# Kernel optimization log

Hardware: AMD Instinct MI355X
Metric: run time of the kernel (lower is better)

The kernel has to match this reference:

```python
import math
import jax, jax.numpy as jnp
import numpy as np

B, CIN, COUT, K, Z, H, W = 8, 512, 512, 3, 512, 64, 64


def setup_inputs() -> dict:
    key = jax.random.key(0)
    k1, k2, k3, k4 = jax.random.split(key, 4)
    inp = {
        "input": jax.random.normal(k1, (B, CIN, H, W), dtype=jnp.float32),
        "style": jax.random.normal(k2, (B, Z), dtype=jnp.float32),
        # base conv weight: [1, out, in, k, k]
        "weight": jax.random.normal(k3, (1, COUT, CIN, K, K), dtype=jnp.float32),
        # EqualLinear modulation params (lr_mul=1, bias_init=1)
        "mod_w": jax.random.normal(k4, (CIN, Z), dtype=jnp.float32),
        "mod_b": jnp.ones((CIN,), dtype=jnp.float32),
    }
    return inp


def reference(input, style, weight, mod_w, mod_b):
    # EqualLinear: scale = 1/sqrt(z_dim), lr_mul = 1, no activation
    z_dim = mod_w.shape[1]
    mod_scale = 1.0 / math.sqrt(z_dim)
    s = style @ (mod_w * mod_scale).T + mod_b  # [B, in]

    # modulated per-sample weights: scale * base_weight * style
    in_ch, k = weight.shape[2], weight.shape[-1]
    conv_scale = 1.0 / math.sqrt(in_ch * k * k)
    w = conv_scale * weight * s[:, None, :, None, None]  # [B, out, in, k, k]

    pad = k // 2

    def conv_one(x, wb):  # x: [in, H, W], wb: [out, in, k, k]
        return jax.lax.conv_general_dilated(
            x[None], wb, window_strides=(1, 1),
            padding=[(pad, pad), (pad, pad)],
            dimension_numbers=("NCHW", "OIHW", "NCHW"),
        )[0]

    out = jax.vmap(conv_one)(input, w)  # [B, out, H, W]
    return out
```

## Files before the change

kernel.cpp:

```cpp
#include <hip/hip_runtime.h>
#include <hip/hip_bf16.h>

#define BB   8
#define CIN  512
#define COUT 512
#define ZD   512
#define HH   64
#define WW   64

#define MOD_SCALE  0.04419417382415922f
#define CONV_SCALE 0.014731391274719742f

typedef __bf16 bf16x8 __attribute__((ext_vector_type(8)));
typedef float  f32x4  __attribute__((ext_vector_type(4)));
typedef float  f32x16 __attribute__((ext_vector_type(16)));

static __device__ __forceinline__ unsigned short f32_to_bf16_rne(float f) {
    unsigned int u = __float_as_uint(f);
    u = (u + 0x7FFFu + ((u >> 16) & 1u)) >> 16;
    return (unsigned short)u;
}

__global__ void k_style(const float* __restrict__ style, const float* __restrict__ mod_w,
                        const float* __restrict__ mod_b, float* __restrict__ sconv) {
    int wid  = blockIdx.x * 4 + (threadIdx.x >> 6);
    int lane = threadIdx.x & 63;
    int b = wid >> 9;
    int i = wid & 511;
    const float4* st = (const float4*)(style + (size_t)b * ZD);
    const float4* mw = (const float4*)(mod_w + (size_t)i * ZD);
    float4 a0 = st[lane],      b0 = mw[lane];
    float4 a1 = st[lane + 64], b1 = mw[lane + 64];
    float sum = a0.x*b0.x + a0.y*b0.y + a0.z*b0.z + a0.w*b0.w
              + a1.x*b1.x + a1.y*b1.y + a1.z*b1.z + a1.w*b1.w;
    #pragma unroll
    for (int off = 32; off > 0; off >>= 1) sum += __shfl_down(sum, off);
    if (lane == 0) sconv[wid] = (sum * MOD_SCALE + mod_b[i]) * CONV_SCALE;
}

__global__ void k_zero_border(unsigned short* __restrict__ xs2p) {
    int b = blockIdx.y;
    int p = blockIdx.x * 4 + (threadIdx.x >> 6);
    int lane = threadIdx.x & 63;
    int h, w;
    if (p < 66)       { h = 0;       w = p; }
    else if (p < 132) { h = 65;      w = p - 66; }
    else if (p < 196) { h = p - 131; w = 0; }
    else              { h = p - 195; w = 65; }
    int4 z = {0, 0, 0, 0};
    *(int4*)&xs2p[((size_t)(b * 66 + h) * 66 + w) * 512 + lane * 8] = z;
}

__global__ void k_scale_input(const float* __restrict__ input, const float* __restrict__ sconv,
                              unsigned short* __restrict__ xs2p) {
    int i0 = blockIdx.x * 32;
    int h  = blockIdx.y;
    int b  = blockIdx.z;
    __shared__ unsigned short lds[64][40];
    #pragma unroll
    for (int r = 0; r < 8; ++r) {
        int ii = r * 4 + (threadIdx.x >> 6);
        int w  = threadIdx.x & 63;
        float v = input[(((size_t)b * CIN + i0 + ii) * HH + h) * WW + w];
        float s = sconv[b * CIN + i0 + ii];
        lds[w][ii] = f32_to_bf16_rne(v * s);
    }
    __syncthreads();
    int w = threadIdx.x >> 2, q = threadIdx.x & 3;
    int4 val = *(const int4*)&lds[w][q * 8];
    *(int4*)&xs2p[((size_t)(b * 66 + h + 1) * 66 + (w + 1)) * 512 + i0 + q * 8] = val;
}

__global__ void k_weight(const float* __restrict__ weight, unsigned short* __restrict__ w3) {
    int t = blockIdx.x * 256 + threadIdx.x;
    int o = t >> 9, i = t & 511;
    int c = i >> 5, g = (i >> 3) & 3, il = i & 7;
    int h = o >> 8, ol = o & 255;
    const float* src = weight + ((size_t)o * CIN + i) * 9;
    #pragma unroll
    for (int p = 0; p < 9; ++p) {
        size_t gran = ((size_t)(c * 9 + p) * 2 + h) * 1024 + g * 256 + ol;
        w3[gran * 8 + il] = f32_to_bf16_rne(src[p]);
    }
}

#define GLD(srcp, ldsbyte)                                                        \
    __builtin_amdgcn_global_load_lds(                                             \
        (const __attribute__((address_space(1))) unsigned int*)(srcp),            \
        (__attribute__((address_space(3))) unsigned int*)(smb + (ldsbyte)),       \
        16, 0, 0)

#define TAP(t, VMA, DOX, DOW) {                                                   \
    const int kh_ = (t) / 3, kw_ = (t) % 3;                                       \
    const int wwr_ = (wrd + 49152) & 65535;                                       \
    if (DOW) { GLD(pW, wwr_ + wdst); GLD(pW + 8192, wwr_ + 8192 + wdst);          \
               pW += 32768; }                                                     \
    if ((DOX) && (t) == 0) { GLD(sxn +  0, xwr + 0 * 8192 + wdst);                \
                             GLD(sxn + 16, xwr + 1 * 8192 + wdst); }              \
    if ((DOX) && (t) == 1) { GLD(sxn + 32, xwr + 2 * 8192 + wdst);                \
                             GLD(sxn + 48, xwr + 3 * 8192 + wdst); }              \
    {   const char* wb = smb + wrd + aoff;                                        \
        const char* xb = smb + xrd + boff + kh_ * 1056 + kw_ * 16;                \
        aA[0] = *(const bf16x8*)(wb);        aA[1] = *(const bf16x8*)(wb + 512);  \
        aA[2] = *(const bf16x8*)(wb + 1024); aA[3] = *(const bf16x8*)(wb + 1536); \
        aB[0] = *(const bf16x8*)(wb + 8192);        aB[1] = *(const bf16x8*)(wb + 8704);  \
        aB[2] = *(const bf16x8*)(wb + 9216);        aB[3] = *(const bf16x8*)(wb + 9728);  \
        bA[0] = *(const bf16x8*)(xb);        bA[1] = *(const bf16x8*)(xb + 512);  \
        bB[0] = *(const bf16x8*)(xb + 16384); bB[1] = *(const bf16x8*)(xb + 16896); \
    }                                                                             \
    asm volatile("s_waitcnt vmcnt(" #VMA ")" ::: "memory");                       \
    __builtin_amdgcn_s_barrier();                                                 \
    asm volatile("s_waitcnt lgkmcnt(0)");                                         \
    __builtin_amdgcn_sched_barrier(0);                                            \
    __builtin_amdgcn_s_setprio(1);                                                \
    _Pragma("unroll") for (int mt = 0; mt < 4; ++mt)                              \
        _Pragma("unroll") for (int nt = 0; nt < 2; ++nt)                          \
            acc[mt][nt] = __builtin_amdgcn_mfma_f32_32x32x16_bf16(                \
                aA[mt], bA[nt], acc[mt][nt], 0, 0, 0);                            \
    _Pragma("unroll") for (int mt = 0; mt < 4; ++mt)                              \
        _Pragma("unroll") for (int nt = 0; nt < 2; ++nt)                          \
            acc[mt][nt] = __builtin_amdgcn_mfma_f32_32x32x16_bf16(                \
                aB[mt], bB[nt], acc[mt][nt], 0, 0, 0);                            \
    __builtin_amdgcn_s_setprio(0);                                                \
    __builtin_amdgcn_s_barrier();                                                 \
    wrd = (wrd + 16384) & 65535;                                                  \
}

__global__ __launch_bounds__(512, 2)
void k_conv(const unsigned short* __restrict__ xs2p, const unsigned short* __restrict__ w3,
            float* __restrict__ out) {
    __shared__ unsigned short smem[65536];
    char* smb = (char*)smem;

    const int tid  = threadIdx.x;
    const int wid  = tid >> 6, lane = tid & 63;
    const int wm   = wid >> 2, wr   = wid & 3;
    const int l31  = lane & 31, l5  = lane >> 5;
    const int half = blockIdx.x;
    const int oc0  = half * 256;
    const int y0   = blockIdx.y * 4;
    const int b    = blockIdx.z;

    const int p_lin = wid * 64 + lane;
    const int xrow  = p_lin / 66;
    const int xcol  = p_lin - xrow * 66;
    const char* srcX = (const char*)xs2p;
    if (p_lin < 396)
        srcX += ((size_t)(b * 66 + y0 + xrow) * 66 + xcol) * 1024;

    const char* pW0 = (const char*)w3 + (size_t)half * 16384 + p_lin * 16;
    const int wdst = p_lin * 16;

    GLD(srcX +  0, 65536 + 0 * 8192 + wdst);
    GLD(srcX + 16, 65536 + 1 * 8192 + wdst);
    GLD(srcX + 32, 65536 + 2 * 8192 + wdst);
    GLD(srcX + 48, 65536 + 3 * 8192 + wdst);
    GLD(pW0,          0     + wdst);
    GLD(pW0 +  8192,  8192  + wdst);
    GLD(pW0 + 32768,  16384 + wdst);
    GLD(pW0 + 40960,  24576 + wdst);
    GLD(pW0 + 65536,  32768 + wdst);
    GLD(pW0 + 73728,  40960 + wdst);
    const char* pW = pW0 + 3 * 32768;
    asm volatile("s_waitcnt vmcnt(4)" ::: "memory");
    __builtin_amdgcn_s_barrier();

    f32x16 acc[4][2];
    #pragma unroll
    for (int mt = 0; mt < 4; ++mt)
        #pragma unroll
        for (int nt = 0; nt < 2; ++nt)
            acc[mt][nt] = (f32x16)(0.f);

    const int aoff = l5 * 4096 + (wm * 128 + l31) * 16;
    const int boff = l5 * 8192 + (wr * 66 + l31) * 16;

    bf16x8 aA[4], aB[4], bA[2], bB[2];
    int wrd = 0;
    int xrd = 65536;
    const char* sxn = srcX + 64;

    for (int c = 0; c < 15; ++c) {
        const int xwr = xrd ^ 32768;
        TAP(0, 6, 1, 1) TAP(1, 8, 1, 1) TAP(2, 8, 0, 1)
        TAP(3, 6, 0, 1) TAP(4, 4, 0, 1) TAP(5, 4, 0, 1)
        TAP(6, 4, 0, 1) TAP(7, 4, 0, 1) TAP(8, 4, 0, 1)
        sxn += 64; xrd ^= 32768;
    }
    {
        const int xwr = 0; (void)xwr;
        TAP(0, 4, 0, 1) TAP(1, 4, 0, 1) TAP(2, 4, 0, 1)
        TAP(3, 4, 0, 1) TAP(4, 4, 0, 1) TAP(5, 4, 0, 1)
        TAP(6, 2, 0, 0) TAP(7, 0, 0, 0) TAP(8, 0, 0, 0)
    }

    const int ybase = (y0 + wr) * 64;
    #pragma unroll
    for (int mt = 0; mt < 4; ++mt)
        #pragma unroll
        for (int nt = 0; nt < 2; ++nt)
            #pragma unroll
            for (int r = 0; r < 16; ++r) {
                int row = (r & 3) + 8 * (r >> 2) + 4 * l5;
                int oc  = oc0 + wm * 128 + mt * 32 + row;
                out[((size_t)(b * COUT + oc) << 12) + ybase + nt * 32 + l31] = acc[mt][nt][r];
            }
}

extern "C" void kernel_launch(void* const* d_in, const int* in_sizes, int n_in,
                              void* d_out, int out_size, void* d_ws, size_t ws_size,
                              hipStream_t stream) {
    const float* input  = (const float*)d_in[0];
    const float* style  = (const float*)d_in[1];
    const float* weight = (const float*)d_in[2];
    const float* mod_w  = (const float*)d_in[3];
    const float* mod_b  = (const float*)d_in[4];
    float* out = (float*)d_out;

    const size_t xs2p_bytes = (size_t)BB * 66 * 66 * 512 * 2;
    const size_t w3_bytes   = (size_t)144 * 2 * 1024 * 8 * 2;
    const size_t need = 16384 + xs2p_bytes + w3_bytes;
    if (ws_size < need) return;

    float*          sconv = (float*)d_ws;
    unsigned short* xs2p  = (unsigned short*)((char*)d_ws + 16384);
    unsigned short* w3    = (unsigned short*)((char*)d_ws + 16384 + xs2p_bytes);

    hipLaunchKernelGGL(k_style,       dim3(1024),      dim3(256), 0, stream, style, mod_w, mod_b, sconv);
    hipLaunchKernelGGL(k_weight,      dim3(1024),      dim3(256), 0, stream, weight, w3);
    hipLaunchKernelGGL(k_zero_border, dim3(65, 8),     dim3(256), 0, stream, xs2p);
    hipLaunchKernelGGL(k_scale_input, dim3(16, 64, 8), dim3(256), 0, stream, input, sconv, xs2p);
    hipLaunchKernelGGL(k_conv,        dim3(2, 16, 8),  dim3(512), 0, stream, xs2p, w3, out);
}
```

Measured before the change: 164.1 us.

## Software-pipeline LDS fragment loads across taps with register double buffering

Splits each tap's operand reads into two halves. The first-half A/B fragments for the next tap are prefetched into alternating E/O register sets while the current tap's MFMAs run. sched_group_barrier interleaves the LDS reads with MFMAs, and each tap now uses one barrier instead of two. This aims to hide LDS latency behind matrix work, at the cost of more registers and tighter vmcnt reasoning about when the prefetched data has landed.

```diff
diff --git a/kernel.cpp b/kernel.cpp
--- a/kernel.cpp
+++ b/kernel.cpp
@@ -90,41 +90,60 @@
         (__attribute__((address_space(3))) unsigned int*)(smb + (ldsbyte)),       \
         16, 0, 0)
 
-#define TAP(t, VMA, DOX, DOW) {                                                   \
-    const int kh_ = (t) / 3, kw_ = (t) % 3;                                       \
+#define TAP(t, VMA, DOX, DOW, DONEXT, C, N) {                                     \
     const int wwr_ = (wrd + 49152) & 65535;                                       \
     if (DOW) { GLD(pW, wwr_ + wdst); GLD(pW + 8192, wwr_ + 8192 + wdst);          \
                pW += 32768; }                                                     \
-    if ((DOX) && (t) == 0) { GLD(sxn +  0, xwr + 0 * 8192 + wdst);                \
-                             GLD(sxn + 16, xwr + 1 * 8192 + wdst); }              \
-    if ((DOX) && (t) == 1) { GLD(sxn + 32, xwr + 2 * 8192 + wdst);                \
-                             GLD(sxn + 48, xwr + 3 * 8192 + wdst); }              \
-    {   const char* wb = smb + wrd + aoff;                                        \
-        const char* xb = smb + xrd + boff + kh_ * 1056 + kw_ * 16;                \
-        aA[0] = *(const bf16x8*)(wb);        aA[1] = *(const bf16x8*)(wb + 512);  \
-        aA[2] = *(const bf16x8*)(wb + 1024); aA[3] = *(const bf16x8*)(wb + 1536); \
-        aB[0] = *(const bf16x8*)(wb + 8192);        aB[1] = *(const bf16x8*)(wb + 8704);  \
-        aB[2] = *(const bf16x8*)(wb + 9216);        aB[3] = *(const bf16x8*)(wb + 9728);  \
-        bA[0] = *(const bf16x8*)(xb);        bA[1] = *(const bf16x8*)(xb + 512);  \
-        bB[0] = *(const bf16x8*)(xb + 16384); bB[1] = *(const bf16x8*)(xb + 16896); \
+    if ((DOX) && (t) == 0) { GLD(sxn +  0, (xrd ^ 32768) + 0 * 8192 + wdst);      \
+                             GLD(sxn + 16, (xrd ^ 32768) + 1 * 8192 + wdst); }    \
+    if ((DOX) && (t) == 1) { GLD(sxn + 32, (xrd ^ 32768) + 2 * 8192 + wdst);      \
+                             GLD(sxn + 48, (xrd ^ 32768) + 3 * 8192 + wdst); }    \
+    {                             \
+      const int kh_ = (t) / 3, kw_ = (t) % 3;                                     \
+      const char* wb1 = smb + wrd + 8192 + aoff;                                  \
+      const char* xb1 = smb + xrd + 16384 + boff + kh_ * 1056 + kw_ * 16;         \
+      a1[0] = *(const bf16x8*)(wb1);         a1[1] = *(const bf16x8*)(wb1 + 512); \
+      a1[2] = *(const bf16x8*)(wb1 + 1024);  a1[3] = *(const bf16x8*)(wb1 + 1536);\
+      b1[0] = *(const bf16x8*)(xb1);         b1[1] = *(const bf16x8*)(xb1 + 512); \
     }                                                                             \
-    asm volatile("s_waitcnt vmcnt(" #VMA ")" ::: "memory");                       \
-    __builtin_amdgcn_s_barrier();                                                 \
-    asm volatile("s_waitcnt lgkmcnt(0)");                                         \
-    __builtin_amdgcn_sched_barrier(0);                                            \
+    if (DONEXT) {                     \
+      const int tn_  = ((t) + 1) % 9;                                             \
+      const int khn_ = tn_ / 3, kwn_ = tn_ % 3;                                   \
+      const int wrdn_ = (wrd + 16384) & 65535;                                    \
+      const int xrdn_ = ((t) == 8) ? (xrd ^ 32768) : xrd;                         \
+      const char* wb0 = smb + wrdn_ + aoff;                                       \
+      const char* xb0 = smb + xrdn_ + boff + khn_ * 1056 + kwn_ * 16;             \
+      a0##N[0] = *(const bf16x8*)(wb0);        a0##N[1] = *(const bf16x8*)(wb0 + 512); \
+      a0##N[2] = *(const bf16x8*)(wb0 + 1024); a0##N[3] = *(const bf16x8*)(wb0 + 1536);\
+      b0##N[0] = *(const bf16x8*)(xb0);        b0##N[1] = *(const bf16x8*)(xb0 + 512); \
+    }                                                                             \
     __builtin_amdgcn_s_setprio(1);                                                \
     _Pragma("unroll") for (int mt = 0; mt < 4; ++mt)                              \
         _Pragma("unroll") for (int nt = 0; nt < 2; ++nt)                          \
             acc[mt][nt] = __builtin_amdgcn_mfma_f32_32x32x16_bf16(                \
-                aA[mt], bA[nt], acc[mt][nt], 0, 0, 0);                            \
+                a0##C[mt], b0##C[nt], acc[mt][nt], 0, 0, 0);                      \
     _Pragma("unroll") for (int mt = 0; mt < 4; ++mt)                              \
         _Pragma("unroll") for (int nt = 0; nt < 2; ++nt)                          \
             acc[mt][nt] = __builtin_amdgcn_mfma_f32_32x32x16_bf16(                \
-                aB[mt], bB[nt], acc[mt][nt], 0, 0, 0);                            \
+                a1[mt], b1[nt], acc[mt][nt], 0, 0, 0);                            \
     __builtin_amdgcn_s_setprio(0);                                                \
+    __builtin_amdgcn_sched_group_barrier(0x100, 3, 0);                            \
+    __builtin_amdgcn_sched_group_barrier(0x008, 4, 0);                            \
+    __builtin_amdgcn_sched_group_barrier(0x100, 3, 0);                            \
+    __builtin_amdgcn_sched_group_barrier(0x008, 4, 0);                            \
+    __builtin_amdgcn_sched_group_barrier(0x100, 3, 0);                            \
+    __builtin_amdgcn_sched_group_barrier(0x008, 4, 0);                            \
+    __builtin_amdgcn_sched_group_barrier(0x100, 3, 0);                            \
+    __builtin_amdgcn_sched_group_barrier(0x008, 4, 0);                            \
+    asm volatile("s_waitcnt vmcnt(" #VMA ")" ::: "memory");                       \
     __builtin_amdgcn_s_barrier();                                                 \
     wrd = (wrd + 16384) & 65535;                                                  \
 }
+
+#define CHUNK_STD(S, N)                                                           \
+    TAP(0, 4, 1, 1, 1, S, N) TAP(1, 4, 1, 1, 1, N, S) TAP(2, 2, 1, 1, 1, S, N)    \
+    TAP(3, 2, 1, 1, 1, N, S) TAP(4, 2, 1, 1, 1, S, N) TAP(5, 2, 1, 1, 1, N, S)    \
+    TAP(6, 2, 1, 1, 1, S, N) TAP(7, 2, 1, 1, 1, N, S) TAP(8, 2, 1, 1, 1, S, N)
 
 __global__ __launch_bounds__(512, 2)
 void k_conv(const unsigned short* __restrict__ xs2p, const unsigned short* __restrict__ w3,
@@ -175,24 +194,27 @@
     const int aoff = l5 * 4096 + (wm * 128 + l31) * 16;
     const int boff = l5 * 8192 + (wr * 66 + l31) * 16;
 
-    bf16x8 aA[4], aB[4], bA[2], bB[2];
+    bf16x8 a0E[4], b0E[2], a0O[4], b0O[2], a1[4], b1[2];
     int wrd = 0;
     int xrd = 65536;
     const char* sxn = srcX + 64;
 
-    for (int c = 0; c < 15; ++c) {
-        const int xwr = xrd ^ 32768;
-        TAP(0, 6, 1, 1) TAP(1, 8, 1, 1) TAP(2, 8, 0, 1)
-        TAP(3, 6, 0, 1) TAP(4, 4, 0, 1) TAP(5, 4, 0, 1)
-        TAP(6, 4, 0, 1) TAP(7, 4, 0, 1) TAP(8, 4, 0, 1)
-        sxn += 64; xrd ^= 32768;
-    }
     {
-        const int xwr = 0; (void)xwr;
-        TAP(0, 4, 0, 1) TAP(1, 4, 0, 1) TAP(2, 4, 0, 1)
-        TAP(3, 4, 0, 1) TAP(4, 4, 0, 1) TAP(5, 4, 0, 1)
-        TAP(6, 2, 0, 0) TAP(7, 0, 0, 0) TAP(8, 0, 0, 0)
-    }
+        const char* wb = smb + aoff;
+        const char* xb = smb + 65536 + boff;
+        a0E[0] = *(const bf16x8*)(wb);         a0E[1] = *(const bf16x8*)(wb + 512);
+        a0E[2] = *(const bf16x8*)(wb + 1024);  a0E[3] = *(const bf16x8*)(wb + 1536);
+        b0E[0] = *(const bf16x8*)(xb);         b0E[1] = *(const bf16x8*)(xb + 512);
+    }
+
+    for (int c2 = 0; c2 < 7; ++c2) {
+        CHUNK_STD(E, O) sxn += 64; xrd ^= 32768;
+        CHUNK_STD(O, E) sxn += 64; xrd ^= 32768;
+    }
+    CHUNK_STD(E, O) sxn += 64; xrd ^= 32768;
+    TAP(0, 2, 0, 1, 1, O, E) TAP(1, 2, 0, 1, 1, E, O) TAP(2, 2, 0, 1, 1, O, E)
+    TAP(3, 2, 0, 1, 1, E, O) TAP(4, 2, 0, 1, 1, O, E) TAP(5, 2, 0, 1, 1, E, O)
+    TAP(6, 0, 0, 0, 1, O, E) TAP(7, 0, 0, 0, 1, E, O) TAP(8, 0, 0, 0, 0, O, E)
 
     const int ybase = (y0 + wr) * 64;
     #pragma unroll
```

Result: no change. 161.9 us (-1.4%).

## Load weights directly to registers and re-tile warps to cut LDS barriers

Applied to the files above, without the earlier changes.

Weight fragments are now read straight from global memory into registers, double-buffered across taps, instead of being staged through LDS with global_load_lds. Only the input tile stays in LDS, which halves shared memory. The per-tap barriers drop to one per input-channel chunk. The warp tiling changes from 2x4 (128 oc × 1 row) to 4x2 (64 oc × 2 rows), which changes how many A and B fragments each warp reuses per tap. The risk is that global-latency weight loads now feed the MFMAs directly with less explicit waiting, and the tap-level pipelining rests on compiler-inserted vmcnt waits.

```diff
diff --git a/kernel.cpp b/kernel.cpp
--- a/kernel.cpp
+++ b/kernel.cpp
@@ -90,51 +90,65 @@
         (__attribute__((address_space(3))) unsigned int*)(smb + (ldsbyte)),       \
         16, 0, 0)
 
-#define TAP(t, VMA, DOX, DOW) {                                                   \
-    const int kh_ = (t) / 3, kw_ = (t) % 3;                                       \
-    const int wwr_ = (wrd + 49152) & 65535;                                       \
-    if (DOW) { GLD(pW, wwr_ + wdst); GLD(pW + 8192, wwr_ + 8192 + wdst);          \
-               pW += 32768; }                                                     \
+#define TAP(t, DOX, DOW, ENDCH, C, N) {                                           \
+    if (DOW) {                                                                    \
+        aW##N[0][0] = *(const bf16x8*)(pA);                                       \
+        aW##N[1][0] = *(const bf16x8*)(pA + 512);                                 \
+        aW##N[0][1] = *(const bf16x8*)(pA + 8192);                                \
+        aW##N[1][1] = *(const bf16x8*)(pA + 8704);                                \
+        pA += 32768;                                                              \
+    }                                                                             \
     if ((DOX) && (t) == 0) { GLD(sxn +  0, xwr + 0 * 8192 + wdst);                \
                              GLD(sxn + 16, xwr + 1 * 8192 + wdst); }              \
     if ((DOX) && (t) == 1) { GLD(sxn + 32, xwr + 2 * 8192 + wdst);                \
                              GLD(sxn + 48, xwr + 3 * 8192 + wdst); }              \
-    {   const char* wb = smb + wrd + aoff;                                        \
-        const char* xb = smb + xrd + boff + kh_ * 1056 + kw_ * 16;                \
-        aA[0] = *(const bf16x8*)(wb);        aA[1] = *(const bf16x8*)(wb + 512);  \
-        aA[2] = *(const bf16x8*)(wb + 1024); aA[3] = *(const bf16x8*)(wb + 1536); \
-        aB[0] = *(const bf16x8*)(wb + 8192);        aB[1] = *(const bf16x8*)(wb + 8704);  \
-        aB[2] = *(const bf16x8*)(wb + 9216);        aB[3] = *(const bf16x8*)(wb + 9728);  \
-        bA[0] = *(const bf16x8*)(xb);        bA[1] = *(const bf16x8*)(xb + 512);  \
-        bB[0] = *(const bf16x8*)(xb + 16384); bB[1] = *(const bf16x8*)(xb + 16896); \
+    {   const int kh_ = (t) / 3, kw_ = (t) % 3;                                   \
+        const char* xb = smb + xrd + boff + (kh_ * 66 + kw_) * 16;                \
+        bfr[0][0] = *(const bf16x8*)(xb);                                         \
+        bfr[1][0] = *(const bf16x8*)(xb + 512);                                   \
+        bfr[2][0] = *(const bf16x8*)(xb + 1056);                                  \
+        bfr[3][0] = *(const bf16x8*)(xb + 1568);                                  \
+        bfr[0][1] = *(const bf16x8*)(xb + 16384);                                 \
+        bfr[1][1] = *(const bf16x8*)(xb + 16896);                                 \
+        bfr[2][1] = *(const bf16x8*)(xb + 17440);                                 \
+        bfr[3][1] = *(const bf16x8*)(xb + 17952);                                 \
     }                                                                             \
-    asm volatile("s_waitcnt vmcnt(" #VMA ")" ::: "memory");                       \
-    __builtin_amdgcn_s_barrier();                                                 \
-    asm volatile("s_waitcnt lgkmcnt(0)");                                         \
-    __builtin_amdgcn_sched_barrier(0);                                            \
     __builtin_amdgcn_s_setprio(1);                                                \
-    _Pragma("unroll") for (int mt = 0; mt < 4; ++mt)                              \
-        _Pragma("unroll") for (int nt = 0; nt < 2; ++nt)                          \
+    _Pragma("unroll") for (int h = 0; h < 2; ++h)                                 \
+      _Pragma("unroll") for (int mt = 0; mt < 2; ++mt)                            \
+        _Pragma("unroll") for (int nt = 0; nt < 4; ++nt)                          \
             acc[mt][nt] = __builtin_amdgcn_mfma_f32_32x32x16_bf16(                \
-                aA[mt], bA[nt], acc[mt][nt], 0, 0, 0);                            \
-    _Pragma("unroll") for (int mt = 0; mt < 4; ++mt)                              \
-        _Pragma("unroll") for (int nt = 0; nt < 2; ++nt)                          \
-            acc[mt][nt] = __builtin_amdgcn_mfma_f32_32x32x16_bf16(                \
-                aB[mt], bB[nt], acc[mt][nt], 0, 0, 0);                            \
+                aW##C[mt][h], bfr[nt][h], acc[mt][nt], 0, 0, 0);                  \
     __builtin_amdgcn_s_setprio(0);                                                \
-    __builtin_amdgcn_s_barrier();                                                 \
-    wrd = (wrd + 16384) & 65535;                                                  \
-}
+    if (ENDCH) { asm volatile("s_waitcnt vmcnt(4)" ::: "memory");                 \
+                 __builtin_amdgcn_s_barrier(); xrd ^= 32768; sxn += 64; }         \
+}
+
+#define CHUNKE_FULL {                                                             \
+    const int xwr = xrd ^ 32768;                                                  \
+    TAP(0, 1, 1, 0, E, O) TAP(1, 1, 1, 0, O, E) TAP(2, 0, 1, 0, E, O)             \
+    TAP(3, 0, 1, 0, O, E) TAP(4, 0, 1, 0, E, O) TAP(5, 0, 1, 0, O, E)             \
+    TAP(6, 0, 1, 0, E, O) TAP(7, 0, 1, 0, O, E) TAP(8, 0, 1, 1, E, O) }
+#define CHUNKO_FULL {                                                             \
+    const int xwr = xrd ^ 32768;                                                  \
+    TAP(0, 1, 1, 0, O, E) TAP(1, 1, 1, 0, E, O) TAP(2, 0, 1, 0, O, E)             \
+    TAP(3, 0, 1, 0, E, O) TAP(4, 0, 1, 0, O, E) TAP(5, 0, 1, 0, E, O)             \
+    TAP(6, 0, 1, 0, O, E) TAP(7, 0, 1, 0, E, O) TAP(8, 0, 1, 1, O, E) }
+#define CHUNKO_TAIL {                                                             \
+    const int xwr = 0; (void)xwr;                                                 \
+    TAP(0, 0, 1, 0, O, E) TAP(1, 0, 1, 0, E, O) TAP(2, 0, 1, 0, O, E)             \
+    TAP(3, 0, 1, 0, E, O) TAP(4, 0, 1, 0, O, E) TAP(5, 0, 1, 0, E, O)             \
+    TAP(6, 0, 1, 0, O, E) TAP(7, 0, 1, 0, E, O) TAP(8, 0, 0, 0, O, E) }
 
 __global__ __launch_bounds__(512, 2)
 void k_conv(const unsigned short* __restrict__ xs2p, const unsigned short* __restrict__ w3,
             float* __restrict__ out) {
-    __shared__ unsigned short smem[65536];
+    __shared__ unsigned short smem[32768];
     char* smb = (char*)smem;
 
     const int tid  = threadIdx.x;
     const int wid  = tid >> 6, lane = tid & 63;
-    const int wm   = wid >> 2, wr   = wid & 3;
+    const int wm4  = wid >> 1, wr2  = wid & 1;
     const int l31  = lane & 31, l5  = lane >> 5;
     const int half = blockIdx.x;
     const int oc0  = half * 256;
@@ -148,63 +162,55 @@
     if (p_lin < 396)
         srcX += ((size_t)(b * 66 + y0 + xrow) * 66 + xcol) * 1024;
 
-    const char* pW0 = (const char*)w3 + (size_t)half * 16384 + p_lin * 16;
+    const char* pA = (const char*)w3 + (size_t)half * 16384
+                   + ((size_t)(l5 * 256 + wm4 * 64 + l31)) * 16;
     const int wdst = p_lin * 16;
 
-    GLD(srcX +  0, 65536 + 0 * 8192 + wdst);
-    GLD(srcX + 16, 65536 + 1 * 8192 + wdst);
-    GLD(srcX + 32, 65536 + 2 * 8192 + wdst);
-    GLD(srcX + 48, 65536 + 3 * 8192 + wdst);
-    GLD(pW0,          0     + wdst);
-    GLD(pW0 +  8192,  8192  + wdst);
-    GLD(pW0 + 32768,  16384 + wdst);
-    GLD(pW0 + 40960,  24576 + wdst);
-    GLD(pW0 + 65536,  32768 + wdst);
-    GLD(pW0 + 73728,  40960 + wdst);
-    const char* pW = pW0 + 3 * 32768;
+    GLD(srcX +  0, 0 * 8192 + wdst);
+    GLD(srcX + 16, 1 * 8192 + wdst);
+    GLD(srcX + 32, 2 * 8192 + wdst);
+    GLD(srcX + 48, 3 * 8192 + wdst);
+    bf16x8 aWE[2][2], aWO[2][2], bfr[4][2];
+    aWE[0][0] = *(const bf16x8*)(pA);
+    aWE[1][0] = *(const bf16x8*)(pA + 512);
+    aWE[0][1] = *(const bf16x8*)(pA + 8192);
+    aWE[1][1] = *(const bf16x8*)(pA + 8704);
+    pA += 32768;
     asm volatile("s_waitcnt vmcnt(4)" ::: "memory");
     __builtin_amdgcn_s_barrier();
 
-    f32x16 acc[4][2];
-    #pragma unroll
-    for (int mt = 0; mt < 4; ++mt)
+    f32x16 acc[2][4];
+    #pragma unroll
+    for (int mt = 0; mt < 2; ++mt)
         #pragma unroll
-        for (int nt = 0; nt < 2; ++nt)
+        for (int nt = 0; nt < 4; ++nt)
             acc[mt][nt] = (f32x16)(0.f);
 
-    const int aoff = l5 * 4096 + (wm * 128 + l31) * 16;
-    const int boff = l5 * 8192 + (wr * 66 + l31) * 16;
-
-    bf16x8 aA[4], aB[4], bA[2], bB[2];
-    int wrd = 0;
-    int xrd = 65536;
+    const int boff = l5 * 8192 + (wr2 * 2 * 66 + l31) * 16;
+
+    int xrd = 0;
     const char* sxn = srcX + 64;
 
-    for (int c = 0; c < 15; ++c) {
-        const int xwr = xrd ^ 32768;
-        TAP(0, 6, 1, 1) TAP(1, 8, 1, 1) TAP(2, 8, 0, 1)
-        TAP(3, 6, 0, 1) TAP(4, 4, 0, 1) TAP(5, 4, 0, 1)
-        TAP(6, 4, 0, 1) TAP(7, 4, 0, 1) TAP(8, 4, 0, 1)
-        sxn += 64; xrd ^= 32768;
+    for (int c2 = 0; c2 < 7; ++c2) {
+        CHUNKE_FULL
+        CHUNKO_FULL
     }
-    {
-        const int xwr = 0; (void)xwr;
-        TAP(0, 4, 0, 1) TAP(1, 4, 0, 1) TAP(2, 4, 0, 1)
-        TAP(3, 4, 0, 1) TAP(4, 4, 0, 1) TAP(5, 4, 0, 1)
-        TAP(6, 2, 0, 0) TAP(7, 0, 0, 0) TAP(8, 0, 0, 0)
-    }
-
-    const int ybase = (y0 + wr) * 64;
-    #pragma unroll
-    for (int mt = 0; mt < 4; ++mt)
+    CHUNKE_FULL
+    CHUNKO_TAIL
+
+    #pragma unroll
+    for (int mt = 0; mt < 2; ++mt)
         #pragma unroll
-        for (int nt = 0; nt < 2; ++nt)
+        for (int nt = 0; nt < 4; ++nt) {
+            const int y  = y0 + wr2 * 2 + (nt >> 1);
+            const int px = (nt & 1) * 32 + l31;
             #pragma unroll
             for (int r = 0; r < 16; ++r) {
                 int row = (r & 3) + 8 * (r >> 2) + 4 * l5;
-                int oc  = oc0 + wm * 128 + mt * 32 + row;
-                out[((size_t)(b * COUT + oc) << 12) + ybase + nt * 32 + l31] = acc[mt][nt][r];
+                int oc  = oc0 + wm4 * 64 + mt * 32 + row;
+                out[((size_t)(b * COUT + oc) << 12) + y * 64 + px] = acc[mt][nt][r];
             }
+        }
 }
 
 extern "C" void kernel_launch(void* const* d_in, const int* in_sizes, int n_in,
```

Result: no change. 167.2 us (+1.9%).

## Shrink conv block tile to 128 output channels for higher occupancy

Applied to the files above, without the earlier changes.

The conv kernel now gives each block 128 output channels instead of 256, with a grid of 16x4x8 and launch bounds raised to 4 blocks per CU. LDS drops to 80KB and the accumulators per wave to 2x2 tiles. The weight buffer moves to a 3-stage ring and the input chunk to a double buffer with a 7168-byte stride. Waits are split per thread group and moved after the MFMAs, so there is one barrier per tap instead of two. The aim is more resident waves to hide memory latency, at the cost of loading each input tile twice as often and less reuse per MFMA.

```diff
diff --git a/kernel.cpp b/kernel.cpp
--- a/kernel.cpp
+++ b/kernel.cpp
@@ -12,7 +12,6 @@
 #define CONV_SCALE 0.014731391274719742f
 
 typedef __bf16 bf16x8 __attribute__((ext_vector_type(8)));
-typedef float  f32x4  __attribute__((ext_vector_type(4)));
 typedef float  f32x16 __attribute__((ext_vector_type(16)));
 
 static __device__ __forceinline__ unsigned short f32_to_bf16_rne(float f) {
@@ -90,121 +89,114 @@
         (__attribute__((address_space(3))) unsigned int*)(smb + (ldsbyte)),       \
         16, 0, 0)
 
-#define TAP(t, VMA, DOX, DOW) {                                                   \
-    const int kh_ = (t) / 3, kw_ = (t) % 3;                                       \
-    const int wwr_ = (wrd + 49152) & 65535;                                       \
-    if (DOW) { GLD(pW, wwr_ + wdst); GLD(pW + 8192, wwr_ + 8192 + wdst);          \
-               pW += 32768; }                                                     \
-    if ((DOX) && (t) == 0) { GLD(sxn +  0, xwr + 0 * 8192 + wdst);                \
-                             GLD(sxn + 16, xwr + 1 * 8192 + wdst); }              \
-    if ((DOX) && (t) == 1) { GLD(sxn + 32, xwr + 2 * 8192 + wdst);                \
-                             GLD(sxn + 48, xwr + 3 * 8192 + wdst); }              \
-    {   const char* wb = smb + wrd + aoff;                                        \
-        const char* xb = smb + xrd + boff + kh_ * 1056 + kw_ * 16;                \
-        aA[0] = *(const bf16x8*)(wb);        aA[1] = *(const bf16x8*)(wb + 512);  \
-        aA[2] = *(const bf16x8*)(wb + 1024); aA[3] = *(const bf16x8*)(wb + 1536); \
-        aB[0] = *(const bf16x8*)(wb + 8192);        aB[1] = *(const bf16x8*)(wb + 8704);  \
-        aB[2] = *(const bf16x8*)(wb + 9216);        aB[3] = *(const bf16x8*)(wb + 9728);  \
-        bA[0] = *(const bf16x8*)(xb);        bA[1] = *(const bf16x8*)(xb + 512);  \
-        bB[0] = *(const bf16x8*)(xb + 16384); bB[1] = *(const bf16x8*)(xb + 16896); \
+#define TAP(t, VMA, VMAW, DOX, DOW) {                                             \
+    const int wwr_ = (wrd >= 8192) ? (wrd - 8192) : 16384;                        \
+    if ((DOX) && (t) < 4 && tid < 448)                                            \
+        GLD(sx + (t) * 16, (xrd ^ 45056) + (t) * 7168 + wdst);                    \
+    if (DOW) { GLD(pW, wwr_ + wdst); pW += 32768; }                               \
+    {   const int ko_ = (((t) / 3) * 66 + ((t) % 3)) * 16;                        \
+        const char* wb = smb + wrd + aoff;                                        \
+        const char* xb = smb + xrd + boff + ko_;                                  \
+        afr[0][0] = *(const bf16x8*)(wb);                                         \
+        afr[0][1] = *(const bf16x8*)(wb + 512);                                   \
+        afr[1][0] = *(const bf16x8*)(wb + 4096);                                  \
+        afr[1][1] = *(const bf16x8*)(wb + 4608);                                  \
+        bfr[0][0] = *(const bf16x8*)(xb);                                         \
+        bfr[0][1] = *(const bf16x8*)(xb + 512);                                   \
+        bfr[1][0] = *(const bf16x8*)(xb + 14336);                                 \
+        bfr[1][1] = *(const bf16x8*)(xb + 14848);                                 \
     }                                                                             \
-    asm volatile("s_waitcnt vmcnt(" #VMA ")" ::: "memory");                       \
-    __builtin_amdgcn_s_barrier();                                                 \
-    asm volatile("s_waitcnt lgkmcnt(0)");                                         \
-    __builtin_amdgcn_sched_barrier(0);                                            \
     __builtin_amdgcn_s_setprio(1);                                                \
-    _Pragma("unroll") for (int mt = 0; mt < 4; ++mt)                              \
+    _Pragma("unroll") for (int h = 0; h < 2; ++h)                                 \
+      _Pragma("unroll") for (int mt = 0; mt < 2; ++mt)                            \
         _Pragma("unroll") for (int nt = 0; nt < 2; ++nt)                          \
             acc[mt][nt] = __builtin_amdgcn_mfma_f32_32x32x16_bf16(                \
-                aA[mt], bA[nt], acc[mt][nt], 0, 0, 0);                            \
-    _Pragma("unroll") for (int mt = 0; mt < 4; ++mt)                              \
-        _Pragma("unroll") for (int nt = 0; nt < 2; ++nt)                          \
-            acc[mt][nt] = __builtin_amdgcn_mfma_f32_32x32x16_bf16(                \
-                aB[mt], bB[nt], acc[mt][nt], 0, 0, 0);                            \
+                afr[h][mt], bfr[h][nt], acc[mt][nt], 0, 0, 0);                    \
     __builtin_amdgcn_s_setprio(0);                                                \
+    if (tid < 448) { asm volatile("s_waitcnt vmcnt(" #VMA ")" ::: "memory"); }    \
+    else           { asm volatile("s_waitcnt vmcnt(" #VMAW ")" ::: "memory"); }   \
     __builtin_amdgcn_s_barrier();                                                 \
-    wrd = (wrd + 16384) & 65535;                                                  \
-}
-
-__global__ __launch_bounds__(512, 2)
+    wrd = (wrd == 16384) ? 0 : (wrd + 8192);                                      \
+}
+
+#define CHUNK_FULL {                                                              \
+    TAP(0, 2, 1, 1, 1) TAP(1, 2, 1, 1, 1) TAP(2, 2, 1, 1, 1) TAP(3, 2, 1, 1, 1)  \
+    TAP(4, 1, 1, 0, 1) TAP(5, 1, 1, 0, 1) TAP(6, 1, 1, 0, 1) TAP(7, 1, 1, 0, 1)  \
+    TAP(8, 1, 1, 0, 1)                                                            \
+    xrd ^= 45056; sx += 64; }
+#define CHUNK_TAIL {                                                              \
+    TAP(0, 1, 1, 0, 1) TAP(1, 1, 1, 0, 1) TAP(2, 1, 1, 0, 1) TAP(3, 1, 1, 0, 1)  \
+    TAP(4, 1, 1, 0, 1) TAP(5, 1, 1, 0, 1) TAP(6, 1, 1, 0, 1)                     \
+    TAP(7, 0, 0, 0, 0) TAP(8, 0, 0, 0, 0) }
+
+__global__ __launch_bounds__(512, 4)
 void k_conv(const unsigned short* __restrict__ xs2p, const unsigned short* __restrict__ w3,
             float* __restrict__ out) {
-    __shared__ unsigned short smem[65536];
+    __shared__ unsigned short smem[40960];
     char* smb = (char*)smem;
 
-    const int tid  = threadIdx.x;
-    const int wid  = tid >> 6, lane = tid & 63;
-    const int wm   = wid >> 2, wr   = wid & 3;
-    const int l31  = lane & 31, l5  = lane >> 5;
-    const int half = blockIdx.x;
-    const int oc0  = half * 256;
-    const int y0   = blockIdx.y * 4;
-    const int b    = blockIdx.z;
-
-    const int p_lin = wid * 64 + lane;
-    const int xrow  = p_lin / 66;
-    const int xcol  = p_lin - xrow * 66;
-    const char* srcX = (const char*)xs2p;
-    if (p_lin < 396)
-        srcX += ((size_t)(b * 66 + y0 + xrow) * 66 + xcol) * 1024;
-
-    const char* pW0 = (const char*)w3 + (size_t)half * 16384 + p_lin * 16;
-    const int wdst = p_lin * 16;
-
-    GLD(srcX +  0, 65536 + 0 * 8192 + wdst);
-    GLD(srcX + 16, 65536 + 1 * 8192 + wdst);
-    GLD(srcX + 32, 65536 + 2 * 8192 + wdst);
-    GLD(srcX + 48, 65536 + 3 * 8192 + wdst);
-    GLD(pW0,          0     + wdst);
-    GLD(pW0 +  8192,  8192  + wdst);
-    GLD(pW0 + 32768,  16384 + wdst);
-    GLD(pW0 + 40960,  24576 + wdst);
-    GLD(pW0 + 65536,  32768 + wdst);
-    GLD(pW0 + 73728,  40960 + wdst);
-    const char* pW = pW0 + 3 * 32768;
-    asm volatile("s_waitcnt vmcnt(4)" ::: "memory");
+    const int tid = threadIdx.x;
+    const int wid = tid >> 6, lane = tid & 63;
+    const int wm  = wid >> 2, wr = wid & 3;
+    const int l31 = lane & 31, l5 = lane >> 5;
+    const int y0  = blockIdx.x * 4;
+    const int ocq = blockIdx.y;
+    const int b   = blockIdx.z;
+
+    const char* sx = (const char*)xs2p;
+    {
+        int slot = tid, r0 = slot / 66, c0 = slot - r0 * 66;
+        if (slot < 396)
+            sx += ((size_t)(b * 66 + y0 + r0) * 66 + c0) * 1024;
+    }
+    const int wdst = tid * 16;
+
+    const char* pW = (const char*)w3 + (size_t)(ocq >> 1) * 16384
+                   + ((size_t)((tid >> 7) * 256 + (ocq & 1) * 128 + (tid & 127))) * 16;
+
+    if (tid < 448) {
+        GLD(sx +  0, 24576 + 0 * 7168 + wdst);
+        GLD(sx + 16, 24576 + 1 * 7168 + wdst);
+        GLD(sx + 32, 24576 + 2 * 7168 + wdst);
+        GLD(sx + 48, 24576 + 3 * 7168 + wdst);
+    }
+    GLD(pW,         0    + wdst);
+    GLD(pW + 32768, 8192 + wdst);
+    pW += 2 * 32768;
+    sx += 64;
+    asm volatile("s_waitcnt vmcnt(1)" ::: "memory");
     __builtin_amdgcn_s_barrier();
 
-    f32x16 acc[4][2];
-    #pragma unroll
-    for (int mt = 0; mt < 4; ++mt)
+    f32x16 acc[2][2];
+    #pragma unroll
+    for (int mt = 0; mt < 2; ++mt)
         #pragma unroll
         for (int nt = 0; nt < 2; ++nt)
             acc[mt][nt] = (f32x16)(0.f);
 
-    const int aoff = l5 * 4096 + (wm * 128 + l31) * 16;
-    const int boff = l5 * 8192 + (wr * 66 + l31) * 16;
-
-    bf16x8 aA[4], aB[4], bA[2], bB[2];
+    const int aoff = l5 * 2048 + (wm * 64 + l31) * 16;
+    const int boff = l5 * 7168 + (wr * 66 + l31) * 16;
+
+    bf16x8 afr[2][2], bfr[2][2];
     int wrd = 0;
-    int xrd = 65536;
-    const char* sxn = srcX + 64;
-
-    for (int c = 0; c < 15; ++c) {
-        const int xwr = xrd ^ 32768;
-        TAP(0, 6, 1, 1) TAP(1, 8, 1, 1) TAP(2, 8, 0, 1)
-        TAP(3, 6, 0, 1) TAP(4, 4, 0, 1) TAP(5, 4, 0, 1)
-        TAP(6, 4, 0, 1) TAP(7, 4, 0, 1) TAP(8, 4, 0, 1)
-        sxn += 64; xrd ^= 32768;
-    }
-    {
-        const int xwr = 0; (void)xwr;
-        TAP(0, 4, 0, 1) TAP(1, 4, 0, 1) TAP(2, 4, 0, 1)
-        TAP(3, 4, 0, 1) TAP(4, 4, 0, 1) TAP(5, 4, 0, 1)
-        TAP(6, 2, 0, 0) TAP(7, 0, 0, 0) TAP(8, 0, 0, 0)
-    }
-
-    const int ybase = (y0 + wr) * 64;
-    #pragma unroll
-    for (int mt = 0; mt < 4; ++mt)
+    int xrd = 24576;
+
+    for (int c = 0; c < 15; ++c) { CHUNK_FULL }
+    CHUNK_TAIL
+
+    const int y = y0 + wr;
+    #pragma unroll
+    for (int mt = 0; mt < 2; ++mt)
         #pragma unroll
-        for (int nt = 0; nt < 2; ++nt)
+        for (int nt = 0; nt < 2; ++nt) {
+            const int px = nt * 32 + l31;
             #pragma unroll
             for (int r = 0; r < 16; ++r) {
                 int row = (r & 3) + 8 * (r >> 2) + 4 * l5;
-                int oc  = oc0 + wm * 128 + mt * 32 + row;
-                out[((size_t)(b * COUT + oc) << 12) + ybase + nt * 32 + l31] = acc[mt][nt][r];
+                int oc  = ocq * 128 + wm * 64 + mt * 32 + row;
+                out[((size_t)(b * COUT + oc) << 12) + y * 64 + px] = acc[mt][nt][r];
             }
+        }
 }
 
 extern "C" void kernel_launch(void* const* d_in, const int* in_sizes, int n_in,
@@ -230,5 +222,5 @@
     hipLaunchKernelGGL(k_weight,      dim3(1024),      dim3(256), 0, stream, weight, w3);
     hipLaunchKernelGGL(k_zero_border, dim3(65, 8),     dim3(256), 0, stream, xs2p);
     hipLaunchKernelGGL(k_scale_input, dim3(16, 64, 8), dim3(256), 0, stream, input, sconv, xs2p);
-    hipLaunchKernelGGL(k_conv,        dim3(2, 16, 8),  dim3(512), 0, stream, xs2p, w3, out);
-}
+    hipLaunchKernelGGL(k_conv,        dim3(16, 4, 8),  dim3(512), 0, stream, xs2p, w3, out);
+}
```

Result: slower. 176.6 us (+7.6%).
